# Kernel tuning notes

Measured on AMD Instinct MI355X. Metric: run time of the kernel, lower is better.

The kernel has to match this reference:

```python
import jax, jax.numpy as jnp
import numpy as np

N = 262144      # total atoms (ragged over batch)
B = 64          # batch_size
K = 16          # retrieved features per sample
H = 256         # h_dim
R = 512         # ret_feat_dim


def setup_inputs() -> dict:
    key = jax.random.key(0)
    k1, k2, k3, k4, k5, k6, k7 = jax.random.split(key, 7)
    h = jax.random.normal(k1, (N, H), dtype=jnp.float32)
    ret_feat = jax.random.normal(k2, (B, K, R), dtype=jnp.float32)
    batch = jnp.sort(jax.random.randint(k3, (N,), 0, B, dtype=jnp.int64))
    # nn.Linear weights: y = x @ W.T + b
    Wp = jax.random.normal(k4, (H, R), dtype=jnp.float32) / np.sqrt(R)
    bp = jax.random.normal(k5, (H,), dtype=jnp.float32) * 0.01
    Wl = jax.random.normal(k6, (H, 2 * H), dtype=jnp.float32) / np.sqrt(2 * H)
    bl = jax.random.normal(k7, (H,), dtype=jnp.float32) * 0.01
    return {"h": h, "ret_feat": ret_feat, "batch": batch,
            "Wp": Wp, "bp": bp, "Wl": Wl, "bl": bl}


def reference(h, ret_feat, batch, Wp, bp, Wl, bl):
    # ret_feat: [B, K, R] -> mean over K -> project to [B, H]
    ret = jnp.mean(ret_feat, axis=1)                    # [B, R]
    ret = ret @ Wp.T + bp                               # [B, H]
    # The torch loop gathers h[batch==i], concats the pooled feature
    # repeated per atom, applies `linear`, and scatters back. Since every
    # atom is covered exactly once, this is a per-node gather + linear:
    per_node = ret[batch]                               # [N, H] gather
    x = jnp.concatenate([h, per_node], axis=-1)         # [N, 2H]
    return x @ Wl.T + bl                                # [N, H]
```

## Files before the change

### kernel.cpp

```cpp
#include <hip/hip_runtime.h>
#include <hip/hip_bf16.h>

#define N_ATOMS 262144
#define B_SZ    64
#define H_DIM   256
#define R_DIM   512

typedef __attribute__((ext_vector_type(8))) short bf16x8;
typedef __attribute__((ext_vector_type(4))) float f32x4;

static __device__ __forceinline__ short f2bf(float f) {
  unsigned u = __builtin_bit_cast(unsigned, f);
  u = (u + 0x7FFFu + ((u >> 16) & 1u)) >> 16;
  return (short)u;
}

__global__ void convert_B_kernel(const float* __restrict__ Wl,
                                 short* __restrict__ Bbf) {
  int idx  = blockIdx.x * 256 + threadIdx.x;
  int j    = idx & 7;
  int lane = (idx >> 3) & 63;
  int ks   = (idx >> 9) & 7;
  int ct   = idx >> 12;
  int o    = ct * 16 + (lane & 15);
  int k    = ks * 32 + ((lane >> 4) << 3) + j;
  Bbf[idx] = f2bf(Wl[o * (2 * H_DIM) + k]);
}

__global__ void pooled_kernel(const float* __restrict__ rf,
                              const float* __restrict__ Wp,
                              const float* __restrict__ bp,
                              const float* __restrict__ Wl,
                              const float* __restrict__ bl,
                              float* __restrict__ pooled) {
  __shared__ float meanr[R_DIM];
  __shared__ float retj[H_DIM];
  int b = blockIdx.x;
  int t = threadIdx.x;

  for (int r = t; r < R_DIM; r += 256) {
    float s = 0.f;
    const float* p = rf + (long)b * 16 * R_DIM + r;
#pragma unroll
    for (int k = 0; k < 16; ++k) s += p[k * R_DIM];
    meanr[r] = s * (1.f / 16.f);
  }
  __syncthreads();

  {
    float s = bp[t];
    const float* w = Wp + (long)t * R_DIM;
    for (int r = 0; r < R_DIM; ++r) s += meanr[r] * w[r];
    retj[t] = s;
  }
  __syncthreads();

  {
    float s = bl[t];
    const float* w = Wl + (long)t * (2 * H_DIM) + H_DIM;
    for (int j = 0; j < H_DIM; ++j) s += retj[j] * w[j];
    pooled[(long)b * H_DIM + t] = s;
  }
}

__global__ __launch_bounds__(1024, 1) void gemm_kernel(
    const float* __restrict__ h, const short* __restrict__ Bbf,
    const float* __restrict__ pooled, const int* __restrict__ batch,
    float* __restrict__ out) {
  __shared__ short As[64 * 256];
  int t    = threadIdx.x;
  int lane = t & 63;
  int w    = t >> 6;
  long m0  = (long)blockIdx.x * 64;

  bf16x8 bfrag[8];
#pragma unroll
  for (int ks = 0; ks < 8; ++ks)
    bfrag[ks] = *(const bf16x8*)(Bbf + (((w * 8 + ks) * 64 + lane) << 3));

  {
    int r  = t >> 4;
    int c0 = (t & 15) << 4;
    const f32x4* src = (const f32x4*)(h + (m0 + r) * H_DIM + c0);
    f32x4 v0 = src[0], v1 = src[1], v2 = src[2], v3 = src[3];
    bf16x8 lo, hi;
    lo[0] = f2bf(v0[0]); lo[1] = f2bf(v0[1]); lo[2] = f2bf(v0[2]); lo[3] = f2bf(v0[3]);
    lo[4] = f2bf(v1[0]); lo[5] = f2bf(v1[1]); lo[6] = f2bf(v1[2]); lo[7] = f2bf(v1[3]);
    hi[0] = f2bf(v2[0]); hi[1] = f2bf(v2[1]); hi[2] = f2bf(v2[2]); hi[3] = f2bf(v2[3]);
    hi[4] = f2bf(v3[0]); hi[5] = f2bf(v3[1]); hi[6] = f2bf(v3[2]); hi[7] = f2bf(v3[3]);
    int base = (r << 9) + (c0 << 1);
    int swz  = (r & 7) << 4;
    *(bf16x8*)((char*)As + ( base        ^ swz)) = lo;
    *(bf16x8*)((char*)As + ((base + 16)  ^ swz)) = hi;
  }
  __syncthreads();

  int o       = (w << 4) + (lane & 15);
  int arow    = lane & 15;
  int kbyte   = (lane >> 4) << 4;
#pragma unroll
  for (int rt = 0; rt < 4; ++rt) {
    f32x4 acc = {0.f, 0.f, 0.f, 0.f};
    int row = rt * 16 + arow;
    int swz = (row & 7) << 4;
#pragma unroll
    for (int ks = 0; ks < 8; ++ks) {
      int off = ((row << 9) + (ks << 6) + kbyte) ^ swz;
      bf16x8 afrag = *(const bf16x8*)((const char*)As + off);
      acc = __builtin_amdgcn_mfma_f32_16x16x32_bf16(afrag, bfrag[ks], acc, 0, 0, 0);
    }
    long rbase = m0 + rt * 16 + ((lane >> 4) << 2);
#pragma unroll
    for (int r = 0; r < 4; ++r) {
      long rowg = rbase + r;
      int  b    = batch[rowg];
      out[rowg * H_DIM + o] = acc[r] + pooled[b * H_DIM + o];
    }
  }
}

extern "C" void kernel_launch(void* const* d_in, const int* in_sizes, int n_in,
                              void* d_out, int out_size, void* d_ws, size_t ws_size,
                              hipStream_t stream) {
  const float* h   = (const float*)d_in[0];
  const float* rf  = (const float*)d_in[1];
  const int*   bat = (const int*)d_in[2];
  const float* Wp  = (const float*)d_in[3];
  const float* bp  = (const float*)d_in[4];
  const float* Wl  = (const float*)d_in[5];
  const float* bl  = (const float*)d_in[6];
  float* out = (float*)d_out;

  float* pooled = (float*)d_ws;
  short* Bbf    = (short*)((char*)d_ws + 64 * 1024);

  convert_B_kernel<<<256, 256, 0, stream>>>(Wl, Bbf);
  pooled_kernel<<<B_SZ, 256, 0, stream>>>(rf, Wp, bp, Wl, bl, pooled);
  gemm_kernel<<<N_ATOMS / 64, 1024, 0, stream>>>(h, Bbf, pooled, bat, out);
}
```

Baseline: 166.5 us.

## Merge prep kernels with warp-parallel dot products and shrink GEMM blocks to 256 threads

Folds the weight-conversion and pooled-feature kernels into one launch. The pooled projections now have each wavefront reduce a row's dot product across lanes with shuffles, so weight reads are coalesced instead of one thread walking a whole row. The GEMM block shrinks from 1024 to 256 threads with up to 4 blocks per CU. Each wave loops over 4 output column tiles and reloads the B fragments for each tile, which aims to improve occupancy and latency hiding at the cost of more B-fragment loads.

```diff
diff --git a/kernel.cpp b/kernel.cpp
--- a/kernel.cpp
+++ b/kernel.cpp
@@ -7,6 +7,7 @@
 #define R_DIM   512
 
 typedef __attribute__((ext_vector_type(8))) short bf16x8;
+typedef __attribute__((ext_vector_type(4))) short bf16x4;
 typedef __attribute__((ext_vector_type(4))) float f32x4;
 
 static __device__ __forceinline__ short f2bf(float f) {
@@ -15,55 +16,75 @@
   return (short)u;
 }
 
-__global__ void convert_B_kernel(const float* __restrict__ Wl,
-                                 short* __restrict__ Bbf) {
-  int idx  = blockIdx.x * 256 + threadIdx.x;
-  int j    = idx & 7;
-  int lane = (idx >> 3) & 63;
-  int ks   = (idx >> 9) & 7;
-  int ct   = idx >> 12;
-  int o    = ct * 16 + (lane & 15);
-  int k    = ks * 32 + ((lane >> 4) << 3) + j;
-  Bbf[idx] = f2bf(Wl[o * (2 * H_DIM) + k]);
-}
+__global__ __launch_bounds__(1024) void prep_kernel(
+    const float* __restrict__ rf, const float* __restrict__ Wp,
+    const float* __restrict__ bp, const float* __restrict__ Wl,
+    const float* __restrict__ bl, float* __restrict__ pooled,
+    short* __restrict__ Bbf) {
+  int t = threadIdx.x;
+  if (blockIdx.x >= B_SZ) {
+    int base = (blockIdx.x - B_SZ) * 4096 + t * 4;
+#pragma unroll
+    for (int q = 0; q < 4; ++q) {
+      int idx  = base + q;
+      int j    = idx & 7;
+      int lane = (idx >> 3) & 63;
+      int ks   = (idx >> 9) & 7;
+      int ct   = idx >> 12;
+      int o    = ct * 16 + (lane & 15);
+      int k    = ks * 32 + ((lane >> 4) << 3) + j;
+      Bbf[idx] = f2bf(Wl[o * (2 * H_DIM) + k]);
+    }
+    return;
+  }
 
-__global__ void pooled_kernel(const float* __restrict__ rf,
-                              const float* __restrict__ Wp,
-                              const float* __restrict__ bp,
-                              const float* __restrict__ Wl,
-                              const float* __restrict__ bl,
-                              float* __restrict__ pooled) {
   __shared__ float meanr[R_DIM];
   __shared__ float retj[H_DIM];
-  int b = blockIdx.x;
-  int t = threadIdx.x;
+  int b    = blockIdx.x;
+  int lane = t & 63;
+  int w    = t >> 6;
 
-  for (int r = t; r < R_DIM; r += 256) {
+  if (t < R_DIM) {
     float s = 0.f;
-    const float* p = rf + (long)b * 16 * R_DIM + r;
+    const float* p = rf + (long)b * 16 * R_DIM + t;
 #pragma unroll
     for (int k = 0; k < 16; ++k) s += p[k * R_DIM];
-    meanr[r] = s * (1.f / 16.f);
+    meanr[t] = s * (1.f / 16.f);
   }
   __syncthreads();
 
   {
-    float s = bp[t];
-    const float* w = Wp + (long)t * R_DIM;
-    for (int r = 0; r < R_DIM; ++r) s += meanr[r] * w[r];
-    retj[t] = s;
+    f32x4 m0 = *(const f32x4*)&meanr[lane * 8];
+    f32x4 m1 = *(const f32x4*)&meanr[lane * 8 + 4];
+#pragma unroll
+    for (int jj = 0; jj < 16; ++jj) {
+      int j = w * 16 + jj;
+      const f32x4* wp = (const f32x4*)(Wp + (long)j * R_DIM + lane * 8);
+      f32x4 w0 = wp[0], w1 = wp[1];
+      float s = m0[0]*w0[0] + m0[1]*w0[1] + m0[2]*w0[2] + m0[3]*w0[3]
+              + m1[0]*w1[0] + m1[1]*w1[1] + m1[2]*w1[2] + m1[3]*w1[3];
+#pragma unroll
+      for (int d = 1; d < 64; d <<= 1) s += __shfl_xor(s, d);
+      if (lane == 0) retj[j] = s + bp[j];
+    }
   }
   __syncthreads();
 
   {
-    float s = bl[t];
-    const float* w = Wl + (long)t * (2 * H_DIM) + H_DIM;
-    for (int j = 0; j < H_DIM; ++j) s += retj[j] * w[j];
-    pooled[(long)b * H_DIM + t] = s;
+    f32x4 r0 = *(const f32x4*)&retj[lane * 4];
+#pragma unroll
+    for (int oo = 0; oo < 16; ++oo) {
+      int o = w * 16 + oo;
+      f32x4 wv = *(const f32x4*)(Wl + (long)o * (2 * H_DIM) + H_DIM + lane * 4);
+      float s = r0[0]*wv[0] + r0[1]*wv[1] + r0[2]*wv[2] + r0[3]*wv[3];
+#pragma unroll
+      for (int d = 1; d < 64; d <<= 1) s += __shfl_xor(s, d);
+      if (lane == 0) pooled[b * H_DIM + o] = s + bl[o];
+    }
   }
 }
 
-__global__ __launch_bounds__(1024, 1) void gemm_kernel(
+__global__ __launch_bounds__(256, 4) void gemm_kernel(
     const float* __restrict__ h, const short* __restrict__ Bbf,
     const float* __restrict__ pooled, const int* __restrict__ batch,
     float* __restrict__ out) {
@@ -73,48 +94,54 @@
   int w    = t >> 6;
   long m0  = (long)blockIdx.x * 64;
 
-  bf16x8 bfrag[8];
+  {
+    const f32x4* src = (const f32x4*)(h + m0 * H_DIM);
 #pragma unroll
-  for (int ks = 0; ks < 8; ++ks)
-    bfrag[ks] = *(const bf16x8*)(Bbf + (((w * 8 + ks) * 64 + lane) << 3));
-
-  {
-    int r  = t >> 4;
-    int c0 = (t & 15) << 4;
-    const f32x4* src = (const f32x4*)(h + (m0 + r) * H_DIM + c0);
-    f32x4 v0 = src[0], v1 = src[1], v2 = src[2], v3 = src[3];
-    bf16x8 lo, hi;
-    lo[0] = f2bf(v0[0]); lo[1] = f2bf(v0[1]); lo[2] = f2bf(v0[2]); lo[3] = f2bf(v0[3]);
-    lo[4] = f2bf(v1[0]); lo[5] = f2bf(v1[1]); lo[6] = f2bf(v1[2]); lo[7] = f2bf(v1[3]);
-    hi[0] = f2bf(v2[0]); hi[1] = f2bf(v2[1]); hi[2] = f2bf(v2[2]); hi[3] = f2bf(v2[3]);
-    hi[4] = f2bf(v3[0]); hi[5] = f2bf(v3[1]); hi[6] = f2bf(v3[2]); hi[7] = f2bf(v3[3]);
-    int base = (r << 9) + (c0 << 1);
-    int swz  = (r & 7) << 4;
-    *(bf16x8*)((char*)As + ( base        ^ swz)) = lo;
-    *(bf16x8*)((char*)As + ((base + 16)  ^ swz)) = hi;
+    for (int i = 0; i < 16; ++i) {
+      int vi = i * 256 + t;
+      f32x4 v = src[vi];
+      bf16x4 bv;
+      bv[0] = f2bf(v[0]); bv[1] = f2bf(v[1]);
+      bv[2] = f2bf(v[2]); bv[3] = f2bf(v[3]);
+      int e   = vi << 2;
+      int row = e >> 8;
+      int col = e & 255;
+      int off = (row << 9) + (col << 1);
+      *(bf16x4*)((char*)As + (off ^ ((row & 7) << 4))) = bv;
+    }
   }
   __syncthreads();
 
-  int o       = (w << 4) + (lane & 15);
-  int arow    = lane & 15;
-  int kbyte   = (lane >> 4) << 4;
+  int arow  = lane & 15;
+  int kbyte = (lane >> 4) << 4;
+  int ocol  = lane & 15;
+
 #pragma unroll
-  for (int rt = 0; rt < 4; ++rt) {
-    f32x4 acc = {0.f, 0.f, 0.f, 0.f};
-    int row = rt * 16 + arow;
-    int swz = (row & 7) << 4;
+  for (int ci = 0; ci < 4; ++ci) {
+    int ct = w * 4 + ci;
+    bf16x8 bfrag[8];
 #pragma unroll
-    for (int ks = 0; ks < 8; ++ks) {
-      int off = ((row << 9) + (ks << 6) + kbyte) ^ swz;
-      bf16x8 afrag = *(const bf16x8*)((const char*)As + off);
-      acc = __builtin_amdgcn_mfma_f32_16x16x32_bf16(afrag, bfrag[ks], acc, 0, 0, 0);
-    }
-    long rbase = m0 + rt * 16 + ((lane >> 4) << 2);
+    for (int ks = 0; ks < 8; ++ks)
+      bfrag[ks] = *(const bf16x8*)(Bbf + (((ct * 8 + ks) * 64 + lane) << 3));
 #pragma unroll
-    for (int r = 0; r < 4; ++r) {
-      long rowg = rbase + r;
-      int  b    = batch[rowg];
-      out[rowg * H_DIM + o] = acc[r] + pooled[b * H_DIM + o];
+    for (int rt = 0; rt < 4; ++rt) {
+      f32x4 acc = {0.f, 0.f, 0.f, 0.f};
+      int row = rt * 16 + arow;
+      int swz = (row & 7) << 4;
+#pragma unroll
+      for (int ks = 0; ks < 8; ++ks) {
+        int off = ((row << 9) + (ks << 6) + kbyte) ^ swz;
+        bf16x8 afrag = *(const bf16x8*)((const char*)As + off);
+        acc = __builtin_amdgcn_mfma_f32_16x16x32_bf16(afrag, bfrag[ks], acc, 0, 0, 0);
+      }
+      long rbase = m0 + rt * 16 + ((lane >> 4) << 2);
+      int  o     = ct * 16 + ocol;
+#pragma unroll
+      for (int r = 0; r < 4; ++r) {
+        long rowg = rbase + r;
+        int  b    = batch[rowg];
+        out[rowg * H_DIM + o] = acc[r] + pooled[b * H_DIM + o];
+      }
     }
   }
 }
@@ -134,7 +161,6 @@
   float* pooled = (float*)d_ws;
   short* Bbf    = (short*)((char*)d_ws + 64 * 1024);
 
-  convert_B_kernel<<<256, 256, 0, stream>>>(Wl, Bbf);
-  pooled_kernel<<<B_SZ, 256, 0, stream>>>(rf, Wp, bp, Wl, bl, pooled);
-  gemm_kernel<<<N_ATOMS / 64, 1024, 0, stream>>>(h, Bbf, pooled, bat, out);
+  prep_kernel<<<B_SZ + 16, 1024, 0, stream>>>(rf, Wp, bp, Wl, bl, pooled, Bbf);
+  gemm_kernel<<<N_ATOMS / 64, 256, 0, stream>>>(h, Bbf, pooled, bat, out);
 }
```

After: 298.1 us. +79.0%, slower.
